# Kernel tuning notes

Measured on AMD Instinct MI355X. Metric: run time of the kernel, lower is better.

## Reference

```python
import jax, jax.numpy as jnp
from jax import lax
import numpy as np

SCALE = 1.0   # self.scale
EPS = 1e-12
CHUNK = 512   # points processed per chunk to bound [P,T,3] temporaries


def _closest_sqdist(p, a, b, c):
    """Squared distance from points p:[P,3] to triangles (a,b,c):[T,3] -> [P,T].
    Ericson's closest-point-on-triangle, fully vectorized."""
    ab = b - a
    ac = c - a
    bc = c - b
    ap = p[:, None, :] - a[None, :, :]
    bp = p[:, None, :] - b[None, :, :]
    cp = p[:, None, :] - c[None, :, :]
    d1 = jnp.einsum('td,ptd->pt', ab, ap)
    d2 = jnp.einsum('td,ptd->pt', ac, ap)
    d3 = jnp.einsum('td,ptd->pt', ab, bp)
    d4 = jnp.einsum('td,ptd->pt', ac, bp)
    d5 = jnp.einsum('td,ptd->pt', ab, cp)
    d6 = jnp.einsum('td,ptd->pt', ac, cp)
    va = d3 * d6 - d5 * d4
    vb = d5 * d2 - d1 * d6
    vc = d1 * d4 - d3 * d2

    def sdiv(n, d):  # NaN/Inf-safe division (branch is masked out by where anyway)
        return n / jnp.where(jnp.abs(d) < EPS, 1.0, d)

    t_ab = sdiv(d1, d1 - d3)[..., None]
    t_ac = sdiv(d2, d2 - d6)[..., None]
    t_bc = sdiv(d4 - d3, (d4 - d3) + (d5 - d6))[..., None]
    denom = va + vb + vc
    v_in = sdiv(vb, denom)[..., None]
    w_in = sdiv(vc, denom)[..., None]

    # base case: interior of the face; then overwrite with edge / vertex regions
    cl = a[None] + v_in * ab[None] + w_in * ac[None]
    cl = jnp.where(((va <= 0) & (d4 - d3 >= 0) & (d5 - d6 >= 0))[..., None],
                   b[None] + t_bc * bc[None], cl)   # edge BC
    cl = jnp.where(((vb <= 0) & (d2 >= 0) & (d6 <= 0))[..., None],
                   a[None] + t_ac * ac[None], cl)   # edge AC
    cl = jnp.where(((vc <= 0) & (d1 >= 0) & (d3 <= 0))[..., None],
                   a[None] + t_ab * ab[None], cl)   # edge AB
    cl = jnp.where(((d6 >= 0) & (d5 <= d6))[..., None], c[None], cl)  # vertex C
    cl = jnp.where(((d3 >= 0) & (d4 <= d3))[..., None], b[None], cl)  # vertex B
    cl = jnp.where(((d1 <= 0) & (d2 <= 0))[..., None], a[None], cl)   # vertex A
    diff = p[:, None, :] - cl
    return jnp.sum(diff * diff, axis=-1)


def setup_inputs():
    key = jax.random.key(0)
    k1, k2, k3 = jax.random.split(key, 3)
    vertices = jax.random.normal(k1, (4, 3, 16, 16, 16), dtype=jnp.float32)
    pc = jax.random.uniform(k2, (4, 4096, 3), dtype=jnp.float32)
    faces = jax.random.randint(k3, (8192, 3), 0, 4096, dtype=jnp.int32)
    return {"vertices": vertices, "pc": pc, "faces": faces}


def reference(vertices, pc, faces):
    B = vertices.shape[0]
    v = jax.nn.sigmoid(vertices)                     # self.normalization
    pos = jnp.moveaxis(v, 1, -1).reshape(B, -1, 3)   # permute(1,2,3,0).view(-1,3)
    pts = pc * SCALE                                 # _scale_points
    # pymesh path drops all-zero points; emulate with a mask (scaling keeps zeros zero)
    mask = jnp.any(pc != 0.0, axis=-1).astype(pts.dtype)  # [B,N]

    def per_batch(args):
        posb, pb, mb = args
        a = posb[faces[:, 0]]
        b = posb[faces[:, 1]]
        c = posb[faces[:, 2]]
        n_chunks = pb.shape[0] // CHUNK

        def chunk_min(pch):  # [CHUNK,3] -> [CHUNK] nearest sq-dist over all tris
            return jnp.min(_closest_sqdist(pch, a, b, c), axis=-1)

        d = lax.map(chunk_min, pb.reshape(n_chunks, CHUNK, 3)).reshape(-1)
        cnt = jnp.maximum(jnp.sum(mb), 1.0)
        return jnp.sum(d * mb) / cnt                 # mean(squared_distances)

    losses = lax.map(per_batch, (pos, pts, mask))    # [B]
    return jnp.mean(losses)
```

## Files before the change

### kernel.cpp

```cpp
#include <hip/hip_runtime.h>
#include <math.h>
#include <float.h>

#define NB 4
#define NP 4096
#define NT 8192
#define TSE 8
#define TEE 20
#define EPSD 1e-12
#define MNS 32
#define MTCH (NT/MNS)
#define NSEED 2048
#define VCH 8
#define VLEN (NSEED/VCH)

__device__ __forceinline__ float sigm(float x) { return 1.0f / (1.0f + expf(-x)); }

__device__ __forceinline__ float tri_dist(
    float px, float py, float pz,
    float ax, float ay, float az,
    float abx, float aby, float abz,
    float acx, float acy, float acz,
    float aa, float am, float cc,
    float raa, float rcc, float rbb,
    float rden, float den, float bb, float k1)
{
  float apx = px - ax, apy = py - ay, apz = pz - az;
  float d1   = apx*abx + apy*aby + apz*abz;
  float d2   = apx*acx + apy*acy + apz*acz;
  float apap = apx*apx + apy*apy + apz*apz;
  float vb = d1*cc - d2*am;
  float vc = d2*aa - d1*am;
  float va = den - vb - vc;
  float di = apap - (vb*d1 + vc*d2)*rden;
  float t2 = d1 + d1;
  float tab = fminf(fmaxf(d1*raa, 0.0f), 1.0f);
  float dAB = apap + tab*(tab*aa - t2);
  float t4 = d2 + d2;
  float tac = fminf(fmaxf(d2*rcc, 0.0f), 1.0f);
  float dAC = apap + tac*(tac*cc - t4);
  float e   = d2 - d1 + k1;
  float tbc = fminf(fmaxf(e*rbb, 0.0f), 1.0f);
  float distB = apap - t2 + aa;
  float dBC = distB + tbc*(tbc*bb - (e + e));
  float m3 = fminf(fminf(dAB, dAC), dBC);
  bool in = (vb >= 0.0f) & (vc >= 0.0f) & (va > 0.0f);
  return in ? di : m3;
}

__global__ __launch_bounds__(256) void prep_kernel(
    const float* __restrict__ verts, const int* __restrict__ faces,
    float* __restrict__ triS, float* __restrict__ triE,
    float* __restrict__ seedA, unsigned* __restrict__ cnt)
{
  int idx = blockIdx.x * 256 + threadIdx.x;
  if (idx == 0) *cnt = 0u;
  if (idx >= NB * NT) return;
  int b = idx >> 13;
  int t = idx & (NT - 1);
  int f0 = faces[3*t + 0], f1 = faces[3*t + 1], f2i = faces[3*t + 2];
  const float* vb_ = verts + (size_t)b * 3 * NP;
  float ax = sigm(vb_[f0]),  ay = sigm(vb_[NP + f0]),  az = sigm(vb_[2*NP + f0]);
  float bx = sigm(vb_[f1]),  by = sigm(vb_[NP + f1]),  bz = sigm(vb_[2*NP + f1]);
  float cx = sigm(vb_[f2i]), cy = sigm(vb_[NP + f2i]), cz = sigm(vb_[2*NP + f2i]);
  float abx = bx - ax, aby = by - ay, abz = bz - az;
  float acx = cx - ax, acy = cy - ay, acz = cz - az;
  double aa = (double)abx*abx + (double)aby*aby + (double)abz*abz;
  double am = (double)abx*acx + (double)aby*acy + (double)abz*acz;
  double cc = (double)acx*acx + (double)acy*acy + (double)acz*acz;
  double den = aa*cc - am*am;
  double bb  = aa - 2.0*am + cc;
  float raa  = (fabs(aa)  < EPSD) ? 1.0f : (float)(1.0/aa);
  float rcc  = (fabs(cc)  < EPSD) ? 1.0f : (float)(1.0/cc);
  float rbb  = (fabs(bb)  < EPSD) ? 1.0f : (float)(1.0/bb);
  float rden = (fabs(den) < EPSD) ? 0.0f : (float)(1.0/den);
  double nx = (double)aby*acz - (double)abz*acy;
  double ny = (double)abz*acx - (double)abx*acz;
  double nz = (double)abx*acy - (double)aby*acx;
  double rs = (fabs(den) < EPSD) ? 0.0 : 1.0 / sqrt(den * 1.02);
  float nhx = (float)(nx * rs), nhy = (float)(ny * rs), nhz = (float)(nz * rs);
  float w = (float)(-(nx*ax + ny*ay + nz*az) * rs);
  float qx = (ax + bx + cx) * (1.0f/3.0f);
  float qy = (ay + by + cy) * (1.0f/3.0f);
  float qz = (az + bz + cz) * (1.0f/3.0f);
  float r2a = (ax-qx)*(ax-qx) + (ay-qy)*(ay-qy) + (az-qz)*(az-qz);
  float r2b = (bx-qx)*(bx-qx) + (by-qy)*(by-qy) + (bz-qz)*(bz-qz);
  float r2c = (cx-qx)*(cx-qx) + (cy-qy)*(cy-qy) + (cz-qz)*(cz-qz);
  float R = sqrtf(fmaxf(r2a, fmaxf(r2b, r2c))) * 1.0005f + 1e-6f;
  float* rs_ = triS + (size_t)idx * TSE;
  rs_[0] = nhx; rs_[1] = nhy; rs_[2] = nhz; rs_[3] = w;
  rs_[4] = qx;  rs_[5] = qy;  rs_[6] = qz;  rs_[7] = R;
  float* re = triE + (size_t)idx * TEE;
  re[0]  = ax;  re[1]  = ay;  re[2]  = az;  re[3]  = abx;
  re[4]  = aby; re[5]  = abz; re[6]  = acx; re[7]  = acy;
  re[8]  = acz; re[9]  = (float)aa; re[10] = (float)am; re[11] = (float)cc;
  re[12] = raa; re[13] = rcc; re[14] = rbb; re[15] = rden;
  re[16] = (float)den; re[17] = (float)bb; re[18] = (float)(aa - am); re[19] = 0.0f;
  if (t < NSEED) {
    float* sa = seedA + (size_t)b * 3 * NSEED + t;
    sa[0] = ax; sa[NSEED] = ay; sa[2*NSEED] = az;
  }
}

__global__ __launch_bounds__(256) void psort_kernel(
    const float* __restrict__ pc, unsigned* __restrict__ perm)
{
  __shared__ unsigned hist[64];
  __shared__ unsigned off[64];
  int b = blockIdx.x;
  int tid = threadIdx.x;
  if (tid < 64) hist[tid] = 0u;
  __syncthreads();
  unsigned cells[16], ranks[16];
  #pragma unroll
  for (int k = 0; k < 16; ++k) {
    int i = k * 256 + tid;
    const float* pp = pc + ((size_t)b * NP + i) * 3;
    float x = pp[0], y = pp[1], z = pp[2];
    int ix = min(3, max(0, (int)(x * 4.0f)));
    int iy = min(3, max(0, (int)(y * 4.0f)));
    int iz = min(3, max(0, (int)(z * 4.0f)));
    unsigned c = (unsigned)(ix | (iy << 2) | (iz << 4));
    cells[k] = c;
    ranks[k] = atomicAdd(&hist[c], 1u);
  }
  __syncthreads();
  if (tid == 0) {
    unsigned acc = 0u;
    for (int c = 0; c < 64; ++c) { off[c] = acc; acc += hist[c]; }
  }
  __syncthreads();
  #pragma unroll
  for (int k = 0; k < 16; ++k) {
    int i = k * 256 + tid;
    perm[(size_t)b * NP + off[cells[k]] + ranks[k]] = (unsigned)i;
  }
}

__global__ __launch_bounds__(256) void seed_kernel(
    const float* __restrict__ seedA, const float* __restrict__ pc,
    float* __restrict__ partS)
{
  int bid  = blockIdx.x;
  int pblk = bid & 15;
  int vc   = (bid >> 4) & (VCH - 1);
  int b    = bid >> 7;
  int p    = pblk * 256 + threadIdx.x;
  const float* pp = pc + ((size_t)b * NP + p) * 3;
  float px = pp[0], py = pp[1], pz = pp[2];
  const float* base = seedA + (size_t)b * 3 * NSEED + vc * VLEN;
  const float4* X = (const float4*)(base);
  const float4* Y = (const float4*)(base + NSEED);
  const float4* Z = (const float4*)(base + 2 * NSEED);
  float m = FLT_MAX;
  #pragma unroll 4
  for (int v = 0; v < VLEN / 4; ++v) {
    float4 vx = X[v], vy = Y[v], vz = Z[v];
    {
      float dx = px - vx.x, dy = py - vy.x, dz = pz - vz.x;
      m = fminf(m, dx*dx + dy*dy + dz*dz);
    }
    {
      float dx = px - vx.y, dy = py - vy.y, dz = pz - vz.y;
      m = fminf(m, dx*dx + dy*dy + dz*dz);
    }
    {
      float dx = px - vx.z, dy = py - vy.z, dz = pz - vz.z;
      m = fminf(m, dx*dx + dy*dy + dz*dz);
    }
    {
      float dx = px - vx.w, dy = py - vy.w, dz = pz - vz.w;
      m = fminf(m, dx*dx + dy*dy + dz*dz);
    }
  }
  partS[((size_t)b * VCH + vc) * NP + p] = m;
}

__global__ __launch_bounds__(256) void main_kernel(
    const float* __restrict__ triS, const float* __restrict__ triE,
    const float* __restrict__ pc, const float* __restrict__ partS,
    const unsigned* __restrict__ perm, float* __restrict__ partM)
{
  __shared__ unsigned qbuf[4][128];
  __shared__ unsigned wmind[4][64];

  int bid  = blockIdx.x;
  int pblk = bid & 15;
  int s    = (bid >> 4) & (MNS - 1);
  int b    = bid >> 9;
  int tid  = threadIdx.x;
  int wave = tid >> 6, lane = tid & 63;
  int p    = (int)perm[(size_t)b * NP + pblk * 256 + tid];

  const float* pp = pc + ((size_t)b * NP + p) * 3;
  float px = pp[0], py = pp[1], pz = pp[2];

  float mind = FLT_MAX;
  #pragma unroll
  for (int j = 0; j < VCH; ++j)
    mind = fminf(mind, partS[((size_t)b * VCH + j) * NP + p]);
  wmind[wave][lane] = __float_as_uint(mind);
  float mth   = mind + 1e-8f;
  float smind = sqrtf(mind) * 1.005f + 1e-5f;

  unsigned qcnt = 0u, qd = 0u;
  const float* triEB = triE + (size_t)b * NT * TEE;
  int tg0 = s * MTCH;
  const float4* Rs = (const float4*)(triS + (size_t)(b * NT + tg0) * TSE);

#define DRAIN_BATCH(NACT)                                                     \
  {                                                                           \
    unsigned ent = qbuf[wave][(qd + (unsigned)lane) & 127u];                  \
    if ((unsigned)lane < (unsigned)(NACT)) {                                  \
      int te  = (int)(ent >> 6);                                              \
      int src = (int)(ent & 63u);                                             \
      float qx = __shfl(px, src, 64);                                         \
      float qy = __shfl(py, src, 64);                                         \
      float qz = __shfl(pz, src, 64);                                         \
      const float* rr = triEB + (size_t)te * TEE;                             \
      float4 w1 = *(const float4*)(rr + 0);                                   \
      float4 w2 = *(const float4*)(rr + 4);                                   \
      float4 w3 = *(const float4*)(rr + 8);                                   \
      float4 w4 = *(const float4*)(rr + 12);                                  \
      float4 w5 = *(const float4*)(rr + 16);                                  \
      float dd = fmaxf(tri_dist(qx, qy, qz,                                   \
                                w1.x, w1.y, w1.z,                             \
                                w1.w, w2.x, w2.y,                             \
                                w2.z, w2.w, w3.x,                             \
                                w3.y, w3.z, w3.w,                             \
                                w4.x, w4.y, w4.z,                             \
                                w4.w, w5.x, w5.y, w5.z), 0.0f);               \
      atomicMin(&wmind[wave][src], __float_as_uint(dd));                      \
    }                                                                         \
    qd += (unsigned)(NACT);                                                   \
    mind  = fminf(mind, __uint_as_float(wmind[wave][lane]));                  \
    mth   = mind + 1e-8f;                                                     \
    smind = sqrtf(mind) * 1.005f + 1e-5f;                                     \
  }

#define SCAN_ITER(Q0, Q1, TIDX)                                               \
  {                                                                           \
    float sN  = fmaf(pz, (Q0).z, fmaf(py, (Q0).y, fmaf(px, (Q0).x, (Q0).w))); \
    float dqx = px - (Q1).x, dqy = py - (Q1).y, dqz = pz - (Q1).z;            \
    float dq2 = fmaf(dqx, dqx, fmaf(dqy, dqy, dqz * dqz));                    \
    float tt  = smind + (Q1).w;                                               \
    bool pred = (sN * sN < mth) & (dq2 < tt * tt);                            \
    unsigned long long mask = __ballot(pred);                                 \
    if (mask) {                                                               \
      if (pred) {                                                             \
        int prefix = __builtin_amdgcn_mbcnt_hi((unsigned)(mask >> 32),        \
                       __builtin_amdgcn_mbcnt_lo((unsigned)mask, 0));         \
        qbuf[wave][(qcnt + (unsigned)prefix) & 127u] =                        \
            ((unsigned)(TIDX) << 6) | (unsigned)lane;                         \
      }                                                                       \
      qcnt += (unsigned)__builtin_popcountll(mask);                           \
      if (qcnt - qd >= 64u) DRAIN_BATCH(64u);                                 \
    }                                                                         \
  }

  float4 a0 = Rs[0], a1 = Rs[1];
  float4 b0 = Rs[2], b1 = Rs[3];
  int tg = tg0;
  for (int g = 0; g < MTCH / 2; ++g) {
    const float4* Rn = Rs + 4;
    float4 c0 = Rn[0], c1 = Rn[1];
    float4 d0 = Rn[2], d1 = Rn[3];
    SCAN_ITER(a0, a1, tg + 0);
    SCAN_ITER(b0, b1, tg + 1);
    a0 = c0; a1 = c1; b0 = d0; b1 = d1;
    Rs = Rn; tg += 2;
  }

  unsigned pend = qcnt - qd;
  if (pend) DRAIN_BATCH(pend);
  mind = fminf(mind, __uint_as_float(wmind[wave][lane]));

  partM[((size_t)b * MNS + s) * NP + p] = fmaxf(mind, 0.0f);

#undef SCAN_ITER
#undef DRAIN_BATCH
}

__global__ __launch_bounds__(256) void reduce_kernel(
    const float* __restrict__ part, const float* __restrict__ pc,
    float* __restrict__ bl2, unsigned* __restrict__ cnt,
    float* __restrict__ out)
{
  int blk = blockIdx.x;
  int b = blk >> 4;
  int p = (blk & 15) * 256 + threadIdx.x;
  float m = FLT_MAX;
  #pragma unroll
  for (int s = 0; s < MNS; ++s)
    m = fminf(m, part[((size_t)b * MNS + s) * NP + p]);
  const float* pp = pc + ((size_t)b * NP + p) * 3;
  float x = pp[0], y = pp[1], z = pp[2];
  float msk = ((x != 0.0f) | (y != 0.0f) | (z != 0.0f)) ? 1.0f : 0.0f;
  float sdm = m * msk, sm = msk;
  for (int off = 32; off > 0; off >>= 1) {
    sdm += __shfl_down(sdm, off, 64);
    sm  += __shfl_down(sm,  off, 64);
  }
  __shared__ float s1[4], s2[4];
  __shared__ bool last;
  int wave = threadIdx.x >> 6, lanei = threadIdx.x & 63;
  if (lanei == 0) { s1[wave] = sdm; s2[wave] = sm; }
  __syncthreads();
  if (threadIdx.x == 0) {
    bl2[2 * blk]     = s1[0] + s1[1] + s1[2] + s1[3];
    bl2[2 * blk + 1] = s2[0] + s2[1] + s2[2] + s2[3];
    __threadfence();
    unsigned t = atomicAdd(cnt, 1u);
    last = (t == 63u);
  }
  __syncthreads();
  if (last) {
    __shared__ float f1[64], f2[64];
    if (threadIdx.x < 64) {
      f1[threadIdx.x] = atomicAdd(&bl2[2 * threadIdx.x],     0.0f);
      f2[threadIdx.x] = atomicAdd(&bl2[2 * threadIdx.x + 1], 0.0f);
    }
    __syncthreads();
    if (threadIdx.x == 0) {
      float acc = 0.0f;
      for (int bb = 0; bb < NB; ++bb) {
        float tsd = 0.0f, tsm = 0.0f;
        for (int k = 0; k < 16; ++k) {
          tsd += f1[bb * 16 + k];
          tsm += f2[bb * 16 + k];
        }
        acc += tsd / fmaxf(tsm, 1.0f);
      }
      out[0] = 0.25f * acc;
    }
  }
}

extern "C" void kernel_launch(void* const* d_in, const int* in_sizes, int n_in,
                              void* d_out, int out_size, void* d_ws, size_t ws_size,
                              hipStream_t stream) {
  const float* verts = (const float*)d_in[0];
  const float* pc    = (const float*)d_in[1];
  const int*   faces = (const int*)d_in[2];
  float* out = (float*)d_out;

  float* triS  = (float*)d_ws;
  float* triE  = triS  + (size_t)NB * NT * TSE;
  float* seedA = triE  + (size_t)NB * NT * TEE;
  float* partS = seedA + (size_t)NB * 3 * NSEED;
  float* partM = partS + (size_t)NB * VCH * NP;
  float* bl2   = partM + (size_t)NB * MNS * NP;
  unsigned* cnt  = (unsigned*)(bl2 + 128);
  unsigned* perm = (unsigned*)(bl2 + 132);

  prep_kernel<<<(NB * NT) / 256, 256, 0, stream>>>(verts, faces, triS, triE, seedA, cnt);
  psort_kernel<<<NB, 256, 0, stream>>>(pc, perm);
  seed_kernel<<<NB * VCH * 16, 256, 0, stream>>>(seedA, pc, partS);
  main_kernel<<<NB * MNS * 16, 256, 0, stream>>>(triS, triE, pc, partS, perm, partM);
  reduce_kernel<<<NB * 16, 256, 0, stream>>>(partM, pc, bl2, cnt, out);
}
```

Baseline: 164.7 us.

## Fuse prep kernels, use AABB culling, dense direct eval, atomicMin partials

Merges the prep, point-sort, seed and init kernels into one launch, so the seed blocks compute sigmoid vertices in LDS themselves. The bounding-sphere cull is replaced by a per-triangle AABB distance test, which makes the triangle record 12 floats wide. When at least 32 lanes pass the cull, the triangle is evaluated directly instead of being queued. Per-slice partial minima are folded into a single per-point buffer with atomicMin, which shrinks the reduce kernel's work. Risks include the AABB test being looser or tighter than the sphere test, extra per-triangle load bandwidth, and atomic contention.

```diff
diff --git a/kernel.cpp b/kernel.cpp
--- a/kernel.cpp
+++ b/kernel.cpp
@@ -5,7 +5,7 @@
 #define NB 4
 #define NP 4096
 #define NT 8192
-#define TSE 8
+#define TSE 12
 #define TEE 20
 #define EPSD 1e-12
 #define MNS 32
@@ -13,6 +13,15 @@
 #define NSEED 2048
 #define VCH 8
 #define VLEN (NSEED/VCH)
+#define DENSE_T 32
+
+#define PREP_BLKS (NB*NT/256)
+#define PSORT_BASE PREP_BLKS
+#define SEED_BASE  (PSORT_BASE + NB)
+#define SEED_BLKS  (NB*VCH*16)
+#define INIT_BASE  (SEED_BASE + SEED_BLKS)
+#define INIT_BLKS  (NB*NP/256)
+#define FUSED_BLKS (INIT_BASE + INIT_BLKS)
 
 __device__ __forceinline__ float sigm(float x) { return 1.0f / (1.0f + expf(-x)); }
 
@@ -48,138 +57,122 @@
   return in ? di : m3;
 }
 
-__global__ __launch_bounds__(256) void prep_kernel(
+__global__ __launch_bounds__(256) void fused_prep_kernel(
     const float* __restrict__ verts, const int* __restrict__ faces,
+    const float* __restrict__ pc,
     float* __restrict__ triS, float* __restrict__ triE,
-    float* __restrict__ seedA, unsigned* __restrict__ cnt)
+    unsigned* __restrict__ perm, float* __restrict__ partS,
+    unsigned* __restrict__ partF, unsigned* __restrict__ cnt)
 {
-  int idx = blockIdx.x * 256 + threadIdx.x;
-  if (idx == 0) *cnt = 0u;
-  if (idx >= NB * NT) return;
-  int b = idx >> 13;
-  int t = idx & (NT - 1);
-  int f0 = faces[3*t + 0], f1 = faces[3*t + 1], f2i = faces[3*t + 2];
-  const float* vb_ = verts + (size_t)b * 3 * NP;
-  float ax = sigm(vb_[f0]),  ay = sigm(vb_[NP + f0]),  az = sigm(vb_[2*NP + f0]);
-  float bx = sigm(vb_[f1]),  by = sigm(vb_[NP + f1]),  bz = sigm(vb_[2*NP + f1]);
-  float cx = sigm(vb_[f2i]), cy = sigm(vb_[NP + f2i]), cz = sigm(vb_[2*NP + f2i]);
-  float abx = bx - ax, aby = by - ay, abz = bz - az;
-  float acx = cx - ax, acy = cy - ay, acz = cz - az;
-  double aa = (double)abx*abx + (double)aby*aby + (double)abz*abz;
-  double am = (double)abx*acx + (double)aby*acy + (double)abz*acz;
-  double cc = (double)acx*acx + (double)acy*acy + (double)acz*acz;
-  double den = aa*cc - am*am;
-  double bb  = aa - 2.0*am + cc;
-  float raa  = (fabs(aa)  < EPSD) ? 1.0f : (float)(1.0/aa);
-  float rcc  = (fabs(cc)  < EPSD) ? 1.0f : (float)(1.0/cc);
-  float rbb  = (fabs(bb)  < EPSD) ? 1.0f : (float)(1.0/bb);
-  float rden = (fabs(den) < EPSD) ? 0.0f : (float)(1.0/den);
-  double nx = (double)aby*acz - (double)abz*acy;
-  double ny = (double)abz*acx - (double)abx*acz;
-  double nz = (double)abx*acy - (double)aby*acx;
-  double rs = (fabs(den) < EPSD) ? 0.0 : 1.0 / sqrt(den * 1.02);
-  float nhx = (float)(nx * rs), nhy = (float)(ny * rs), nhz = (float)(nz * rs);
-  float w = (float)(-(nx*ax + ny*ay + nz*az) * rs);
-  float qx = (ax + bx + cx) * (1.0f/3.0f);
-  float qy = (ay + by + cy) * (1.0f/3.0f);
-  float qz = (az + bz + cz) * (1.0f/3.0f);
-  float r2a = (ax-qx)*(ax-qx) + (ay-qy)*(ay-qy) + (az-qz)*(az-qz);
-  float r2b = (bx-qx)*(bx-qx) + (by-qy)*(by-qy) + (bz-qz)*(bz-qz);
-  float r2c = (cx-qx)*(cx-qx) + (cy-qy)*(cy-qy) + (cz-qz)*(cz-qz);
-  float R = sqrtf(fmaxf(r2a, fmaxf(r2b, r2c))) * 1.0005f + 1e-6f;
-  float* rs_ = triS + (size_t)idx * TSE;
-  rs_[0] = nhx; rs_[1] = nhy; rs_[2] = nhz; rs_[3] = w;
-  rs_[4] = qx;  rs_[5] = qy;  rs_[6] = qz;  rs_[7] = R;
-  float* re = triE + (size_t)idx * TEE;
-  re[0]  = ax;  re[1]  = ay;  re[2]  = az;  re[3]  = abx;
-  re[4]  = aby; re[5]  = abz; re[6]  = acx; re[7]  = acy;
-  re[8]  = acz; re[9]  = (float)aa; re[10] = (float)am; re[11] = (float)cc;
-  re[12] = raa; re[13] = rcc; re[14] = rbb; re[15] = rden;
-  re[16] = (float)den; re[17] = (float)bb; re[18] = (float)(aa - am); re[19] = 0.0f;
-  if (t < NSEED) {
-    float* sa = seedA + (size_t)b * 3 * NSEED + t;
-    sa[0] = ax; sa[NSEED] = ay; sa[2*NSEED] = az;
-  }
-}
-
-__global__ __launch_bounds__(256) void psort_kernel(
-    const float* __restrict__ pc, unsigned* __restrict__ perm)
-{
-  __shared__ unsigned hist[64];
-  __shared__ unsigned off[64];
-  int b = blockIdx.x;
+  int blk = blockIdx.x;
   int tid = threadIdx.x;
-  if (tid < 64) hist[tid] = 0u;
-  __syncthreads();
-  unsigned cells[16], ranks[16];
-  #pragma unroll
-  for (int k = 0; k < 16; ++k) {
-    int i = k * 256 + tid;
-    const float* pp = pc + ((size_t)b * NP + i) * 3;
-    float x = pp[0], y = pp[1], z = pp[2];
-    int ix = min(3, max(0, (int)(x * 4.0f)));
-    int iy = min(3, max(0, (int)(y * 4.0f)));
-    int iz = min(3, max(0, (int)(z * 4.0f)));
-    unsigned c = (unsigned)(ix | (iy << 2) | (iz << 4));
-    cells[k] = c;
-    ranks[k] = atomicAdd(&hist[c], 1u);
-  }
-  __syncthreads();
-  if (tid == 0) {
-    unsigned acc = 0u;
-    for (int c = 0; c < 64; ++c) { off[c] = acc; acc += hist[c]; }
-  }
-  __syncthreads();
-  #pragma unroll
-  for (int k = 0; k < 16; ++k) {
-    int i = k * 256 + tid;
-    perm[(size_t)b * NP + off[cells[k]] + ranks[k]] = (unsigned)i;
-  }
-}
-
-__global__ __launch_bounds__(256) void seed_kernel(
-    const float* __restrict__ seedA, const float* __restrict__ pc,
-    float* __restrict__ partS)
-{
-  int bid  = blockIdx.x;
-  int pblk = bid & 15;
-  int vc   = (bid >> 4) & (VCH - 1);
-  int b    = bid >> 7;
-  int p    = pblk * 256 + threadIdx.x;
-  const float* pp = pc + ((size_t)b * NP + p) * 3;
-  float px = pp[0], py = pp[1], pz = pp[2];
-  const float* base = seedA + (size_t)b * 3 * NSEED + vc * VLEN;
-  const float4* X = (const float4*)(base);
-  const float4* Y = (const float4*)(base + NSEED);
-  const float4* Z = (const float4*)(base + 2 * NSEED);
-  float m = FLT_MAX;
-  #pragma unroll 4
-  for (int v = 0; v < VLEN / 4; ++v) {
-    float4 vx = X[v], vy = Y[v], vz = Z[v];
-    {
-      float dx = px - vx.x, dy = py - vy.x, dz = pz - vz.x;
+
+  if (blk < PREP_BLKS) {
+    if (blk == 0 && tid == 0) *cnt = 0u;
+    int idx = blk * 256 + tid;
+    int b = idx >> 13;
+    int t = idx & (NT - 1);
+    int f0 = faces[3*t + 0], f1 = faces[3*t + 1], f2i = faces[3*t + 2];
+    const float* vb_ = verts + (size_t)b * 3 * NP;
+    float ax = sigm(vb_[f0]),  ay = sigm(vb_[NP + f0]),  az = sigm(vb_[2*NP + f0]);
+    float bx = sigm(vb_[f1]),  by = sigm(vb_[NP + f1]),  bz = sigm(vb_[2*NP + f1]);
+    float cx = sigm(vb_[f2i]), cy = sigm(vb_[NP + f2i]), cz = sigm(vb_[2*NP + f2i]);
+    float abx = bx - ax, aby = by - ay, abz = bz - az;
+    float acx = cx - ax, acy = cy - ay, acz = cz - az;
+    double aa = (double)abx*abx + (double)aby*aby + (double)abz*abz;
+    double am = (double)abx*acx + (double)aby*acy + (double)abz*acz;
+    double cc = (double)acx*acx + (double)acy*acy + (double)acz*acz;
+    double den = aa*cc - am*am;
+    double bb  = aa - 2.0*am + cc;
+    float raa  = (fabs(aa)  < EPSD) ? 1.0f : (float)(1.0/aa);
+    float rcc  = (fabs(cc)  < EPSD) ? 1.0f : (float)(1.0/cc);
+    float rbb  = (fabs(bb)  < EPSD) ? 1.0f : (float)(1.0/bb);
+    float rden = (fabs(den) < EPSD) ? 0.0f : (float)(1.0/den);
+    double nx = (double)aby*acz - (double)abz*acy;
+    double ny = (double)abz*acx - (double)abx*acz;
+    double nz = (double)abx*acy - (double)aby*acx;
+    double rs = (fabs(den) < EPSD) ? 0.0 : 1.0 / sqrt(den * 1.02);
+    float nhx = (float)(nx * rs), nhy = (float)(ny * rs), nhz = (float)(nz * rs);
+    float w = (float)(-(nx*ax + ny*ay + nz*az) * rs);
+    float lox = fminf(ax, fminf(bx, cx)), hix = fmaxf(ax, fmaxf(bx, cx));
+    float loy = fminf(ay, fminf(by, cy)), hiy = fmaxf(ay, fmaxf(by, cy));
+    float loz = fminf(az, fminf(bz, cz)), hiz = fmaxf(az, fmaxf(bz, cz));
+    float* rs_ = triS + (size_t)idx * TSE;
+    rs_[0] = nhx; rs_[1] = nhy; rs_[2]  = nhz;  rs_[3]  = w;
+    rs_[4] = lox; rs_[5] = loy; rs_[6]  = loz;  rs_[7]  = hix;
+    rs_[8] = hiy; rs_[9] = hiz; rs_[10] = 0.0f; rs_[11] = 0.0f;
+    float* re = triE + (size_t)idx * TEE;
+    re[0]  = ax;  re[1]  = ay;  re[2]  = az;  re[3]  = abx;
+    re[4]  = aby; re[5]  = abz; re[6]  = acx; re[7]  = acy;
+    re[8]  = acz; re[9]  = (float)aa; re[10] = (float)am; re[11] = (float)cc;
+    re[12] = raa; re[13] = rcc; re[14] = rbb; re[15] = rden;
+    re[16] = (float)den; re[17] = (float)bb; re[18] = (float)(aa - am); re[19] = 0.0f;
+
+  } else if (blk < SEED_BASE) {
+    __shared__ unsigned hist[64];
+    __shared__ unsigned off[64];
+    int b = blk - PSORT_BASE;
+    if (tid < 64) hist[tid] = 0u;
+    __syncthreads();
+    unsigned cells[16], ranks[16];
+    #pragma unroll
+    for (int k = 0; k < 16; ++k) {
+      int i = k * 256 + tid;
+      const float* pp = pc + ((size_t)b * NP + i) * 3;
+      float x = pp[0], y = pp[1], z = pp[2];
+      int ix = min(3, max(0, (int)(x * 4.0f)));
+      int iy = min(3, max(0, (int)(y * 4.0f)));
+      int iz = min(3, max(0, (int)(z * 4.0f)));
+      unsigned c = (unsigned)(ix | (iy << 2) | (iz << 4));
+      cells[k] = c;
+      ranks[k] = atomicAdd(&hist[c], 1u);
+    }
+    __syncthreads();
+    if (tid == 0) {
+      unsigned acc = 0u;
+      for (int c = 0; c < 64; ++c) { off[c] = acc; acc += hist[c]; }
+    }
+    __syncthreads();
+    #pragma unroll
+    for (int k = 0; k < 16; ++k) {
+      int i = k * 256 + tid;
+      perm[(size_t)b * NP + off[cells[k]] + ranks[k]] = (unsigned)i;
+    }
+
+  } else if (blk < INIT_BASE) {
+    __shared__ float sx[VLEN], sy[VLEN], sz[VLEN];
+    int sid  = blk - SEED_BASE;
+    int pblk = sid & 15;
+    int vc   = (sid >> 4) & (VCH - 1);
+    int b    = sid >> 7;
+    int t    = vc * VLEN + tid;
+    int f0   = faces[3 * t];
+    const float* vb_ = verts + (size_t)b * 3 * NP;
+    sx[tid] = sigm(vb_[f0]);
+    sy[tid] = sigm(vb_[NP + f0]);
+    sz[tid] = sigm(vb_[2 * NP + f0]);
+    __syncthreads();
+    int p = pblk * 256 + tid;
+    const float* pp = pc + ((size_t)b * NP + p) * 3;
+    float px = pp[0], py = pp[1], pz = pp[2];
+    float m = FLT_MAX;
+    #pragma unroll 4
+    for (int j = 0; j < VLEN; ++j) {
+      float dx = px - sx[j], dy = py - sy[j], dz = pz - sz[j];
       m = fminf(m, dx*dx + dy*dy + dz*dz);
     }
-    {
-      float dx = px - vx.y, dy = py - vy.y, dz = pz - vz.y;
-      m = fminf(m, dx*dx + dy*dy + dz*dz);
-    }
-    {
-      float dx = px - vx.z, dy = py - vy.z, dz = pz - vz.z;
-      m = fminf(m, dx*dx + dy*dy + dz*dz);
-    }
-    {
-      float dx = px - vx.w, dy = py - vy.w, dz = pz - vz.w;
-      m = fminf(m, dx*dx + dy*dy + dz*dz);
-    }
-  }
-  partS[((size_t)b * VCH + vc) * NP + p] = m;
+    partS[((size_t)b * VCH + vc) * NP + p] = m;
+
+  } else {
+    int i = (blk - INIT_BASE) * 256 + tid;
+    partF[i] = 0x7F7FFFFFu;
+  }
 }
 
 __global__ __launch_bounds__(256) void main_kernel(
     const float* __restrict__ triS, const float* __restrict__ triE,
     const float* __restrict__ pc, const float* __restrict__ partS,
-    const unsigned* __restrict__ perm, float* __restrict__ partM)
+    const unsigned* __restrict__ perm, unsigned* __restrict__ partF)
 {
   __shared__ unsigned qbuf[4][128];
   __shared__ unsigned wmind[4][64];
@@ -200,8 +193,7 @@
   for (int j = 0; j < VCH; ++j)
     mind = fminf(mind, partS[((size_t)b * VCH + j) * NP + p]);
   wmind[wave][lane] = __float_as_uint(mind);
-  float mth   = mind + 1e-8f;
-  float smind = sqrtf(mind) * 1.005f + 1e-5f;
+  float mth = mind + 1e-8f;
 
   unsigned qcnt = 0u, qd = 0u;
   const float* triEB = triE + (size_t)b * NT * TEE;
@@ -233,41 +225,61 @@
       atomicMin(&wmind[wave][src], __float_as_uint(dd));                      \
     }                                                                         \
     qd += (unsigned)(NACT);                                                   \
-    mind  = fminf(mind, __uint_as_float(wmind[wave][lane]));                  \
-    mth   = mind + 1e-8f;                                                     \
-    smind = sqrtf(mind) * 1.005f + 1e-5f;                                     \
-  }
-
-#define SCAN_ITER(Q0, Q1, TIDX)                                               \
+    mind = fminf(mind, __uint_as_float(wmind[wave][lane]));                   \
+    mth  = mind + 1e-8f;                                                      \
+  }
+
+#define SCAN_ITER(Q0, Q1, Q2, TIDX)                                           \
   {                                                                           \
-    float sN  = fmaf(pz, (Q0).z, fmaf(py, (Q0).y, fmaf(px, (Q0).x, (Q0).w))); \
-    float dqx = px - (Q1).x, dqy = py - (Q1).y, dqz = pz - (Q1).z;            \
-    float dq2 = fmaf(dqx, dqx, fmaf(dqy, dqy, dqz * dqz));                    \
-    float tt  = smind + (Q1).w;                                               \
-    bool pred = (sN * sN < mth) & (dq2 < tt * tt);                            \
+    float sN = fmaf(pz, (Q0).z, fmaf(py, (Q0).y, fmaf(px, (Q0).x, (Q0).w)));  \
+    float dx = fmaxf(fmaxf((Q1).x - px, px - (Q1).w), 0.0f);                  \
+    float dy = fmaxf(fmaxf((Q1).y - py, py - (Q2).x), 0.0f);                  \
+    float dz = fmaxf(fmaxf((Q1).z - pz, pz - (Q2).y), 0.0f);                  \
+    float bb2 = fmaf(dx, dx, fmaf(dy, dy, dz * dz));                          \
+    bool pred = (sN * sN < mth) & (bb2 * 0.98f < mth);                        \
     unsigned long long mask = __ballot(pred);                                 \
     if (mask) {                                                               \
-      if (pred) {                                                             \
-        int prefix = __builtin_amdgcn_mbcnt_hi((unsigned)(mask >> 32),        \
-                       __builtin_amdgcn_mbcnt_lo((unsigned)mask, 0));         \
-        qbuf[wave][(qcnt + (unsigned)prefix) & 127u] =                        \
-            ((unsigned)(TIDX) << 6) | (unsigned)lane;                         \
+      int nsv = __builtin_popcountll(mask);                                   \
+      if (nsv >= DENSE_T) {                                                   \
+        const float* rr = triEB + (size_t)(TIDX) * TEE;                       \
+        float4 w1 = *(const float4*)(rr + 0);                                 \
+        float4 w2 = *(const float4*)(rr + 4);                                 \
+        float4 w3 = *(const float4*)(rr + 8);                                 \
+        float4 w4 = *(const float4*)(rr + 12);                                \
+        float4 w5 = *(const float4*)(rr + 16);                                \
+        float dd = fmaxf(tri_dist(px, py, pz,                                 \
+                                  w1.x, w1.y, w1.z,                           \
+                                  w1.w, w2.x, w2.y,                           \
+                                  w2.z, w2.w, w3.x,                           \
+                                  w3.y, w3.z, w3.w,                           \
+                                  w4.x, w4.y, w4.z,                           \
+                                  w4.w, w5.x, w5.y, w5.z), 0.0f);             \
+        mind = fminf(mind, dd);                                               \
+        mth  = mind + 1e-8f;                                                  \
+      } else {                                                                \
+        if (pred) {                                                           \
+          int prefix = __builtin_amdgcn_mbcnt_hi((unsigned)(mask >> 32),      \
+                         __builtin_amdgcn_mbcnt_lo((unsigned)mask, 0));       \
+          qbuf[wave][(qcnt + (unsigned)prefix) & 127u] =                      \
+              ((unsigned)(TIDX) << 6) | (unsigned)lane;                       \
+        }                                                                     \
+        qcnt += (unsigned)nsv;                                                \
+        if (qcnt - qd >= 64u) DRAIN_BATCH(64u);                               \
       }                                                                       \
-      qcnt += (unsigned)__builtin_popcountll(mask);                           \
-      if (qcnt - qd >= 64u) DRAIN_BATCH(64u);                                 \
     }                                                                         \
   }
 
-  float4 a0 = Rs[0], a1 = Rs[1];
-  float4 b0 = Rs[2], b1 = Rs[3];
+  float4 a0 = Rs[0], a1 = Rs[1], a2 = Rs[2];
+  float4 b0 = Rs[3], b1 = Rs[4], b2 = Rs[5];
   int tg = tg0;
   for (int g = 0; g < MTCH / 2; ++g) {
-    const float4* Rn = Rs + 4;
-    float4 c0 = Rn[0], c1 = Rn[1];
-    float4 d0 = Rn[2], d1 = Rn[3];
-    SCAN_ITER(a0, a1, tg + 0);
-    SCAN_ITER(b0, b1, tg + 1);
-    a0 = c0; a1 = c1; b0 = d0; b1 = d1;
+    const float4* Rn = Rs + 6;
+    float4 c0 = Rn[0], c1 = Rn[1], c2 = Rn[2];
+    float4 d0 = Rn[3], d1 = Rn[4], d2 = Rn[5];
+    SCAN_ITER(a0, a1, a2, tg + 0);
+    SCAN_ITER(b0, b1, b2, tg + 1);
+    a0 = c0; a1 = c1; a2 = c2;
+    b0 = d0; b1 = d1; b2 = d2;
     Rs = Rn; tg += 2;
   }
 
@@ -275,24 +287,21 @@
   if (pend) DRAIN_BATCH(pend);
   mind = fminf(mind, __uint_as_float(wmind[wave][lane]));
 
-  partM[((size_t)b * MNS + s) * NP + p] = fmaxf(mind, 0.0f);
+  atomicMin(&partF[(size_t)b * NP + p], __float_as_uint(fmaxf(mind, 0.0f)));
 
 #undef SCAN_ITER
 #undef DRAIN_BATCH
 }
 
 __global__ __launch_bounds__(256) void reduce_kernel(
-    const float* __restrict__ part, const float* __restrict__ pc,
+    const float* __restrict__ partF, const float* __restrict__ pc,
     float* __restrict__ bl2, unsigned* __restrict__ cnt,
     float* __restrict__ out)
 {
   int blk = blockIdx.x;
   int b = blk >> 4;
   int p = (blk & 15) * 256 + threadIdx.x;
-  float m = FLT_MAX;
-  #pragma unroll
-  for (int s = 0; s < MNS; ++s)
-    m = fminf(m, part[((size_t)b * MNS + s) * NP + p]);
+  float m = partF[(size_t)b * NP + p];
   const float* pp = pc + ((size_t)b * NP + p) * 3;
   float x = pp[0], y = pp[1], z = pp[2];
   float msk = ((x != 0.0f) | (y != 0.0f) | (z != 0.0f)) ? 1.0f : 0.0f;
@@ -346,16 +355,15 @@
 
   float* triS  = (float*)d_ws;
   float* triE  = triS  + (size_t)NB * NT * TSE;
-  float* seedA = triE  + (size_t)NB * NT * TEE;
-  float* partS = seedA + (size_t)NB * 3 * NSEED;
-  float* partM = partS + (size_t)NB * VCH * NP;
-  float* bl2   = partM + (size_t)NB * MNS * NP;
+  float* partS = triE  + (size_t)NB * NT * TEE;
+  float* partF = partS + (size_t)NB * VCH * NP;
+  float* bl2   = partF + (size_t)NB * NP;
   unsigned* cnt  = (unsigned*)(bl2 + 128);
   unsigned* perm = (unsigned*)(bl2 + 132);
 
-  prep_kernel<<<(NB * NT) / 256, 256, 0, stream>>>(verts, faces, triS, triE, seedA, cnt);
-  psort_kernel<<<NB, 256, 0, stream>>>(pc, perm);
-  seed_kernel<<<NB * VCH * 16, 256, 0, stream>>>(seedA, pc, partS);
-  main_kernel<<<NB * MNS * 16, 256, 0, stream>>>(triS, triE, pc, partS, perm, partM);
-  reduce_kernel<<<NB * 16, 256, 0, stream>>>(partM, pc, bl2, cnt, out);
-}
+  fused_prep_kernel<<<FUSED_BLKS, 256, 0, stream>>>(
+      verts, faces, pc, triS, triE, perm, partS, (unsigned*)partF, cnt);
+  main_kernel<<<NB * MNS * 16, 256, 0, stream>>>(
+      triS, triE, pc, partS, perm, (unsigned*)partF);
+  reduce_kernel<<<NB * 16, 256, 0, stream>>>(partF, pc, bl2, cnt, out);
+}
```

Measured after the change: 190.4 us. 1.16x slower.
